# Optimization experiments

Hardware: AMD Instinct MI355X
Metric: run time of the kernel (lower is better)

## Reference

```python
import jax, jax.numpy as jnp
import numpy as np

DT = 0.01
DX = 1.0
DY = 1.0
NUM_STEPS = 10


def _diff(a, axis, h):
    """Central difference in the interior, one-sided at boundaries, along `axis`.
    a: [B, H, W]; returns same shape."""
    def sl(s):
        idx = [slice(None)] * a.ndim
        idx[axis] = s
        return a[tuple(idx)]
    left = (sl(slice(1, 2)) - sl(slice(0, 1))) / h            # one-sided forward at boundary 0
    interior = (sl(slice(2, None)) - sl(slice(None, -2))) / (2.0 * h)
    right = (sl(slice(-1, None)) - sl(slice(-2, -1))) / h     # one-sided backward at boundary -1
    return jnp.concatenate([left, interior, right], axis=axis)


def _diffusion_step(u, alpha, beta, aniso_x, aniso_y):
    # u: [B, H, W]; axis 1 = y, axis 2 = x (matches torch indexing)
    grad_x = _diff(u, axis=2, h=DX)
    grad_y = _diff(u, axis=1, h=DY)
    flux_x = (alpha * aniso_x) * grad_x   # scalars broadcast
    flux_y = (beta * aniso_y) * grad_y
    div_flux = _diff(flux_x, axis=2, h=DX) + _diff(flux_y, axis=1, h=DY)
    return u + DT * div_flux


def setup_inputs() -> dict:
    key = jax.random.key(0)
    k1, = jax.random.split(key, 1)
    u = jax.random.normal(k1, (64, 1, 512, 512), dtype=jnp.float32)
    ones = jnp.ones((1,), dtype=jnp.float32)
    return {
        "u": u,
        "alpha": ones * 0.5,
        "beta": ones * 0.5,
        "aniso_x": ones,
        "aniso_y": ones,
        "edge_strength": ones * 0.1,
    }


def reference(u, alpha, beta, aniso_x, aniso_y, edge_strength):
    # u: [B, 1, H, W] -> squeeze channel
    x = u[:, 0]                       # [B, H, W]
    x_orig = x

    def body(carry, _):
        return _diffusion_step(carry, alpha, beta, aniso_x, aniso_y), None

    x, _ = jax.lax.scan(body, x, None, length=NUM_STEPS)
    alpha_mix = jax.nn.sigmoid(edge_strength)   # shape (1,), broadcasts
    out = alpha_mix * x + (1.0 - alpha_mix) * x_orig
    return out[:, None]               # [B, 1, H, W]
```

## Files before the change

### kernel.cpp

```cpp
#include <hip/hip_runtime.h>
#include <math.h>

#define W 512
#define H 512
#define IMG (W * H)
#define LSTRIDE 84
#define WWORDS 2560
#define LWORDS (4 * WWORDS)

__host__ __device__ constexpr double dcoefd(int i, int j) {
    if (i == 0) return j == 0 ? 0.5 : j == 1 ? -1.0 : j == 2 ? 0.5 : 0.0;
    if (i == 1) return j == 0 ? 0.5 : j == 1 ? -0.75 : j == 3 ? 0.25 : 0.0;
    return j == i - 2 ? 0.25 : j == i ? -0.5 : j == i + 2 ? 0.25 : 0.0;
}

struct GhostT {
    float g[7][8];
    constexpr GhostT() : g{} {
        double v0[8] = {}, v1[8] = {}, v2[8] = {}, w0[8] = {}, w1r[8] = {}, w2r[8] = {};
        for (int j = 0; j < 8; ++j) { v0[j] = dcoefd(0, j); v1[j] = dcoefd(1, j); v2[j] = dcoefd(2, j); }
        for (int j = 0; j < 8; ++j) {
            double s0 = 0, s1 = 0, s2 = 0;
            for (int k = 0; k < 10; ++k) {
                s0 += dcoefd(0, k) * dcoefd(k, j);
                s1 += dcoefd(1, k) * dcoefd(k, j);
                s2 += dcoefd(2, k) * dcoefd(k, j);
            }
            w0[j] = s0; w1r[j] = s1; w2r[j] = s2;
        }
        double um1[8] = {}, um2[8] = {}, um3[8] = {}, um4[8] = {}, um5[8] = {}, um6[8] = {};
        double vm1[8] = {}, vm2[8] = {}, vm3[8] = {}, vm4[8] = {}, wm1[8] = {}, wm2[8] = {};
        for (int j = 0; j < 8; ++j) {
            um1[j] = 2.0 * (j == 0) - (j == 1);
            um2[j] = 4.0 * (j == 0) - 4.0 * (j == 1) + (j == 2);
            vm1[j] = 2 * v0[j] - v1[j];
            vm2[j] = 4 * v0[j] - 4 * v1[j] + v2[j];
            wm1[j] = 2 * w0[j] - w1r[j];
            wm2[j] = 4 * w0[j] - 4 * w1r[j] + w2r[j];
        }
        for (int j = 0; j < 8; ++j) {
            um3[j] = 4 * vm1[j] + 2 * um1[j] - (j == 1);
            um4[j] = 4 * vm2[j] + 2 * um2[j] - (j == 0);
            vm3[j] = 4 * wm1[j] + 2 * vm1[j] - v1[j];
            vm4[j] = 4 * wm2[j] + 2 * vm2[j] - v0[j];
        }
        for (int j = 0; j < 8; ++j) {
            um5[j] = 4 * vm3[j] + 2 * um3[j] - um1[j];
            um6[j] = 4 * vm4[j] + 2 * um4[j] - um2[j];
        }
        for (int j = 0; j < 8; ++j) {
            g[1][j] = (float)um1[j]; g[2][j] = (float)um2[j]; g[3][j] = (float)um3[j];
            g[4][j] = (float)um4[j]; g[5][j] = (float)um5[j]; g[6][j] = (float)um6[j];
        }
    }
};
constexpr GhostT GH{};

__device__ __forceinline__ float4 ld4(const float* p) {
    return *reinterpret_cast<const float4*>(p);
}
__device__ __forceinline__ float rfl(float x) {
    return __int_as_float(__builtin_amdgcn_readfirstlane(__float_as_int(x)));
}

struct Uni {
    float k1, k2, k3, m1, m2, n1;
    float wy1a, wy1b, wy2a, wy2b, wy2c, wy3a, wy3b, wy3c, wy3d;
    float am, iam;
};

template<int CLS, int RI>
__device__ __forceinline__ void row_lds(const Uni& U, const float* __restrict__ lbase,
                                        float acc[4][4]) {
    const float* rowp = lbase + 2 * RI * LSTRIDE;
    float u0a[4], t1a[4], t2a[4], t3a[4];
    if (CLS == 0) {
        const float4 m2 = ld4(rowp + 8);
        u0a[0] = m2.x; u0a[1] = m2.y; u0a[2] = m2.z; u0a[3] = m2.w;
    } else if (CLS <= 2) {
        const float4 m1 = ld4(rowp + 4);
        const float4 m2 = ld4(rowp + 8);
        const float4 m3 = ld4(rowp + 12);
        u0a[0] = m2.x; u0a[1] = m2.y; u0a[2] = m2.z; u0a[3] = m2.w;
        t1a[0] = m1.z + m2.z; t1a[1] = m1.w + m2.w;
        t1a[2] = m2.x + m3.x; t1a[3] = m2.y + m3.y;
        t2a[0] = m1.x + m3.x; t2a[1] = m1.y + m3.y;
        t2a[2] = m1.z + m3.z; t2a[3] = m1.w + m3.w;
    } else {
        const float4 m0 = ld4(rowp);
        const float4 m4 = ld4(rowp + 16);
        const float4 m1 = ld4(rowp + 4);
        const float4 m3 = ld4(rowp + 12);
        t3a[0] = m0.z + m3.z; t3a[1] = m0.w + m3.w;
        t3a[2] = m1.x + m4.x; t3a[3] = m1.y + m4.y;
        t2a[0] = m1.x + m3.x; t2a[1] = m1.y + m3.y;
        t2a[2] = m1.z + m3.z; t2a[3] = m1.w + m3.w;
        const float4 m2 = ld4(rowp + 8);
        t1a[0] = m1.z + m2.z; t1a[1] = m1.w + m2.w;
        t1a[2] = m2.x + m3.x; t1a[3] = m2.y + m3.y;
        u0a[0] = m2.x; u0a[1] = m2.y; u0a[2] = m2.z; u0a[3] = m2.w;
    }

    #pragma unroll
    for (int j = 0; j < 4; ++j) {
        const float u0 = u0a[j];
        const float M3v = 120.f * u0;
        float M2v = 0.f, M1v = 0.f, M0v = 0.f;
        if (CLS >= 1) {
            const float X1 = fmaf(0.25f, t1a[j], -0.5f * u0);
            M2v = fmaf(U.n1, X1, 45.f * u0);
            if (CLS >= 2) {
                const float X2 = fmaf(0.0625f, t2a[j], fmaf(-0.25f, t1a[j], 0.375f * u0));
                M1v = fmaf(U.m1, X1, fmaf(U.m2, X2, 10.f * u0));
                if (CLS >= 3) {
                    const float X3 = fmaf(1.f/64, t3a[j], fmaf(-6.f/64, t2a[j],
                                      fmaf(15.f/64, t1a[j], (-20.f/64) * u0)));
                    M0v = fmaf(U.k1, X1, fmaf(U.k2, X2, U.k3 * X3));
                }
            }
        }
        #pragma unroll
        for (int k = 0; k < 4; ++k) {
            const int dq = RI - 3 - k;
            const int ad = dq < 0 ? -dq : dq;
            if (ad > 3) continue;
            float a = acc[k][j];
            if (ad == 0) {
                a = fmaf(U.iam, u0, a);
                a += M0v;
                a = fmaf(U.wy1b, M1v, a);
                a = fmaf(U.wy2c, M2v, a);
                a = fmaf(U.wy3d, M3v, a);
            } else if (ad == 1) {
                a = fmaf(U.wy1a, M1v, a);
                a = fmaf(U.wy2b, M2v, a);
                a = fmaf(U.wy3c, M3v, a);
            } else if (ad == 2) {
                a = fmaf(U.wy2a, M2v, a);
                a = fmaf(U.wy3b, M3v, a);
            } else {
                a = fmaf(U.wy3a, M3v, a);
            }
            acc[k][j] = a;
        }
    }
}

__global__ __launch_bounds__(256) void fused_v17(
        const float* __restrict__ uin, float* __restrict__ outp,
        const float* __restrict__ alpha, const float* __restrict__ beta,
        const float* __restrict__ axp, const float* __restrict__ ayp,
        const float* __restrict__ es) {
    __shared__ float lds0[LWORDS];

    const unsigned bid = blockIdx.x;
    const unsigned swz = (bid & 7u) * (gridDim.x >> 3) + (bid >> 3);
    const unsigned img  = swz >> 6;
    const unsigned tile = swz & 63u;
    const int gx0 = (int)(tile & 7u) << 6;
    const int gy0 = (int)(tile >> 3) << 6;
    const float* __restrict__ p = uin + (size_t)img * IMG;
    float* __restrict__ q = outp + (size_t)img * IMG;

    const int tid = threadIdx.x;
    const int wid = tid >> 6, lane = tid & 63;
    const int WB = wid * WWORDS;
    const int wrow0 = 16 * wid - 6;

    #pragma unroll
    for (int t = 0; t < 10; ++t) {
        int idx = (t << 8) + (lane << 2);
        int lr  = (int)((unsigned)idx / 84u);
        int col = idx - lr * 84;
        int gy = gy0 + wrow0 + lr;
        gy = gy < 0 ? 0 : (gy > H - 1 ? H - 1 : gy);
        int gx = gx0 + col - 8;
        gx = gx < 0 ? 0 : (gx > W - 4 ? W - 4 : gx);
        const float* src = p + (size_t)gy * W + gx;
        __builtin_amdgcn_global_load_lds(
            (const __attribute__((address_space(1))) void*)src,
            (__attribute__((address_space(3))) void*)&lds0[WB + idx],
            16, 0, 0);
    }
    asm volatile("s_waitcnt vmcnt(0)" ::: "memory");

    if (gy0 == 0 && wid == 0 && lane < 20) {
        const int w0 = lane << 2;
        #pragma unroll
        for (int k = 1; k <= 6; ++k) {
            float4 a = {0.f, 0.f, 0.f, 0.f};
            #pragma unroll
            for (int j = 0; j < 8; ++j) {
                const float w = GH.g[k][j];
                if (w != 0.f) {
                    const float4 r = ld4(&lds0[WB + (6 + j) * LSTRIDE + w0]);
                    a.x = fmaf(w, r.x, a.x); a.y = fmaf(w, r.y, a.y);
                    a.z = fmaf(w, r.z, a.z); a.w = fmaf(w, r.w, a.w);
                }
            }
            *reinterpret_cast<float4*>(&lds0[WB + (6 - k) * LSTRIDE + w0]) = a;
        }
    }
    if (gy0 == H - 64 && wid == 3 && lane < 20) {
        const int w0 = lane << 2;
        #pragma unroll
        for (int k = 1; k <= 6; ++k) {
            float4 a = {0.f, 0.f, 0.f, 0.f};
            #pragma unroll
            for (int j = 0; j < 8; ++j) {
                const float w = GH.g[k][j];
                if (w != 0.f) {
                    const float4 r = ld4(&lds0[WB + (21 - j) * LSTRIDE + w0]);
                    a.x = fmaf(w, r.x, a.x); a.y = fmaf(w, r.y, a.y);
                    a.z = fmaf(w, r.z, a.z); a.w = fmaf(w, r.w, a.w);
                }
            }
            *reinterpret_cast<float4*>(&lds0[WB + (21 + k) * LSTRIDE + w0]) = a;
        }
    }

    if ((gx0 == 0 || gx0 == W - 64) && lane < 28) {
        float* rp = &lds0[WB + lane * LSTRIDE];
        #pragma unroll
        for (int k = 1; k <= 6; ++k) {
            float s = 0.f;
            #pragma unroll
            for (int j = 0; j < 8; ++j) {
                const float w = GH.g[k][j];
                if (w != 0.f) {
                    const float v = (gx0 == 0) ? rp[8 + j] : rp[71 - j];
                    s = fmaf(w, v, s);
                }
            }
            if (gx0 == 0) rp[8 - k] = s; else rp[71 + k] = s;
        }
    }

    const float sx = 0.01f * alpha[0] * axp[0];
    const float sy = 0.01f * beta[0]  * ayp[0];
    Uni U;
    U.k1 = rfl(10.f * sx);  U.k2 = rfl(45.f * sx * sx);  U.k3 = rfl(120.f * sx * sx * sx);
    U.m1 = rfl(90.f * sx);  U.m2 = rfl(360.f * sx * sx); U.n1 = rfl(360.f * sx);
    const float sy2 = sy * sy, sy3 = sy2 * sy;
    U.wy1a = rfl(0.25f * sy);    U.wy1b = rfl(-0.5f * sy);
    U.wy2a = rfl(0.0625f * sy2); U.wy2b = rfl(-0.25f * sy2); U.wy2c = rfl(0.375f * sy2);
    U.wy3a = rfl((1.f/64) * sy3);  U.wy3b = rfl((-6.f/64) * sy3);
    U.wy3c = rfl((15.f/64) * sy3); U.wy3d = rfl((-20.f/64) * sy3);
    const float amv = 1.f / (1.f + expf(-es[0]));
    U.am = rfl(amv); U.iam = rfl(1.f / amv);

    const int qc = tid & 15;
    const int gw = (tid >> 4) & 3;
    const int ly0 = ((gw >> 1) << 3) + (gw & 1);
    const int x0 = qc << 2;
    const float* lbase = &lds0[WB + ly0 * LSTRIDE + x0];

    float acc[4][4] = {};
    row_lds<0, 0>(U, lbase, acc);
    row_lds<1, 1>(U, lbase, acc);
    row_lds<2, 2>(U, lbase, acc);
    row_lds<3, 3>(U, lbase, acc);
    row_lds<3, 4>(U, lbase, acc);
    row_lds<3, 5>(U, lbase, acc);
    row_lds<3, 6>(U, lbase, acc);
    row_lds<2, 7>(U, lbase, acc);
    row_lds<1, 8>(U, lbase, acc);
    row_lds<0, 9>(U, lbase, acc);

    const int ybase = gy0 + 16 * wid + ly0;
    #pragma unroll
    for (int k = 0; k < 4; ++k) {
        const int Yo = ybase + 2 * k;
        float4 o;
        o.x = U.am * acc[k][0];
        o.y = U.am * acc[k][1];
        o.z = U.am * acc[k][2];
        o.w = U.am * acc[k][3];
        *reinterpret_cast<float4*>(q + (size_t)Yo * W + gx0 + x0) = o;
    }
}

extern "C" void kernel_launch(void* const* d_in, const int* in_sizes, int n_in,
                              void* d_out, int out_size, void* d_ws, size_t ws_size,
                              hipStream_t stream) {
    const float* u     = (const float*)d_in[0];
    const float* alpha = (const float*)d_in[1];
    const float* beta  = (const float*)d_in[2];
    const float* ax    = (const float*)d_in[3];
    const float* ay    = (const float*)d_in[4];
    const float* es    = (const float*)d_in[5];
    float* out = (float*)d_out;

    int nimg = in_sizes[0] / IMG;
    dim3 block(256);
    dim3 grid((unsigned)(nimg * 64));
    fused_v17<<<grid, block, 0, stream>>>(u, out, alpha, beta, ax, ay, es);
}
```

Before: 34.13 us.

## Process two horizontal tiles per block with double-buffered LDS staging

```diff
diff --git a/kernel.cpp b/kernel.cpp
--- a/kernel.cpp
+++ b/kernel.cpp
@@ -6,7 +6,7 @@
 #define IMG (W * H)
 #define LSTRIDE 84
 #define WWORDS 2560
-#define LWORDS (4 * WWORDS)
+#define LWORDS (8 * WWORDS)
 
 __host__ __device__ constexpr double dcoefd(int i, int j) {
     if (i == 0) return j == 0 ? 0.5 : j == 1 ? -1.0 : j == 2 ? 0.5 : 0.0;
@@ -146,27 +146,9 @@
     }
 }
 
-__global__ __launch_bounds__(256) void fused_v17(
-        const float* __restrict__ uin, float* __restrict__ outp,
-        const float* __restrict__ alpha, const float* __restrict__ beta,
-        const float* __restrict__ axp, const float* __restrict__ ayp,
-        const float* __restrict__ es) {
-    __shared__ float lds0[LWORDS];
-
-    const unsigned bid = blockIdx.x;
-    const unsigned swz = (bid & 7u) * (gridDim.x >> 3) + (bid >> 3);
-    const unsigned img  = swz >> 6;
-    const unsigned tile = swz & 63u;
-    const int gx0 = (int)(tile & 7u) << 6;
-    const int gy0 = (int)(tile >> 3) << 6;
-    const float* __restrict__ p = uin + (size_t)img * IMG;
-    float* __restrict__ q = outp + (size_t)img * IMG;
-
-    const int tid = threadIdx.x;
-    const int wid = tid >> 6, lane = tid & 63;
-    const int WB = wid * WWORDS;
-    const int wrow0 = 16 * wid - 6;
-
+__device__ __forceinline__ void stage_wave(const float* __restrict__ p,
+                                           float* ldsb, int gy0, int gx0,
+                                           int wrow0, int lane) {
     #pragma unroll
     for (int t = 0; t < 10; ++t) {
         int idx = (t << 8) + (lane << 2);
@@ -179,11 +161,13 @@
         const float* src = p + (size_t)gy * W + gx;
         __builtin_amdgcn_global_load_lds(
             (const __attribute__((address_space(1))) void*)src,
-            (__attribute__((address_space(3))) void*)&lds0[WB + idx],
+            (__attribute__((address_space(3))) void*)&ldsb[idx],
             16, 0, 0);
     }
-    asm volatile("s_waitcnt vmcnt(0)" ::: "memory");
-
+}
+
+__device__ __forceinline__ void ghost_wave(float* ldsb, int gy0, int gx0,
+                                           int wid, int lane) {
     if (gy0 == 0 && wid == 0 && lane < 20) {
         const int w0 = lane << 2;
         #pragma unroll
@@ -193,12 +177,12 @@
             for (int j = 0; j < 8; ++j) {
                 const float w = GH.g[k][j];
                 if (w != 0.f) {
-                    const float4 r = ld4(&lds0[WB + (6 + j) * LSTRIDE + w0]);
+                    const float4 r = ld4(&ldsb[(6 + j) * LSTRIDE + w0]);
                     a.x = fmaf(w, r.x, a.x); a.y = fmaf(w, r.y, a.y);
                     a.z = fmaf(w, r.z, a.z); a.w = fmaf(w, r.w, a.w);
                 }
             }
-            *reinterpret_cast<float4*>(&lds0[WB + (6 - k) * LSTRIDE + w0]) = a;
+            *reinterpret_cast<float4*>(&ldsb[(6 - k) * LSTRIDE + w0]) = a;
         }
     }
     if (gy0 == H - 64 && wid == 3 && lane < 20) {
@@ -210,17 +194,16 @@
             for (int j = 0; j < 8; ++j) {
                 const float w = GH.g[k][j];
                 if (w != 0.f) {
-                    const float4 r = ld4(&lds0[WB + (21 - j) * LSTRIDE + w0]);
+                    const float4 r = ld4(&ldsb[(21 - j) * LSTRIDE + w0]);
                     a.x = fmaf(w, r.x, a.x); a.y = fmaf(w, r.y, a.y);
                     a.z = fmaf(w, r.z, a.z); a.w = fmaf(w, r.w, a.w);
                 }
             }
-            *reinterpret_cast<float4*>(&lds0[WB + (21 + k) * LSTRIDE + w0]) = a;
-        }
-    }
-
+            *reinterpret_cast<float4*>(&ldsb[(21 + k) * LSTRIDE + w0]) = a;
+        }
+    }
     if ((gx0 == 0 || gx0 == W - 64) && lane < 28) {
-        float* rp = &lds0[WB + lane * LSTRIDE];
+        float* rp = &ldsb[lane * LSTRIDE];
         #pragma unroll
         for (int k = 1; k <= 6; ++k) {
             float s = 0.f;
@@ -235,6 +218,64 @@
             if (gx0 == 0) rp[8 - k] = s; else rp[71 + k] = s;
         }
     }
+}
+
+__device__ __forceinline__ void compute_wave(const Uni& U, const float* ldsb,
+                                             float* __restrict__ q,
+                                             int gy0, int gx0, int wid, int tid) {
+    const int qc = tid & 15;
+    const int gw = (tid >> 4) & 3;
+    const int ly0 = ((gw >> 1) << 3) + (gw & 1);
+    const int x0 = qc << 2;
+    const float* lbase = &ldsb[ly0 * LSTRIDE + x0];
+
+    float acc[4][4] = {};
+    row_lds<0, 0>(U, lbase, acc);
+    row_lds<1, 1>(U, lbase, acc);
+    row_lds<2, 2>(U, lbase, acc);
+    row_lds<3, 3>(U, lbase, acc);
+    row_lds<3, 4>(U, lbase, acc);
+    row_lds<3, 5>(U, lbase, acc);
+    row_lds<3, 6>(U, lbase, acc);
+    row_lds<2, 7>(U, lbase, acc);
+    row_lds<1, 8>(U, lbase, acc);
+    row_lds<0, 9>(U, lbase, acc);
+
+    const int ybase = gy0 + 16 * wid + ly0;
+    #pragma unroll
+    for (int k = 0; k < 4; ++k) {
+        const int Yo = ybase + 2 * k;
+        float4 o;
+        o.x = U.am * acc[k][0];
+        o.y = U.am * acc[k][1];
+        o.z = U.am * acc[k][2];
+        o.w = U.am * acc[k][3];
+        *reinterpret_cast<float4*>(q + (size_t)Yo * W + gx0 + x0) = o;
+    }
+}
+
+__global__ __launch_bounds__(256) void fused_v18(
+        const float* __restrict__ uin, float* __restrict__ outp,
+        const float* __restrict__ alpha, const float* __restrict__ beta,
+        const float* __restrict__ axp, const float* __restrict__ ayp,
+        const float* __restrict__ es) {
+    __shared__ float lds0[LWORDS];
+
+    const unsigned bid = blockIdx.x;
+    const unsigned swz = (bid & 7u) * (gridDim.x >> 3) + (bid >> 3);
+    const unsigned img = swz >> 5;
+    const unsigned pr  = swz & 31u;
+    const int gy0 = (int)(pr >> 2) << 6;
+    const int gxA = (int)(pr & 3u) << 7;
+    const int gxB = gxA + 64;
+    const float* __restrict__ p = uin + (size_t)img * IMG;
+    float* __restrict__ q = outp + (size_t)img * IMG;
+
+    const int tid = threadIdx.x;
+    const int wid = tid >> 6, lane = tid & 63;
+    const int wrow0 = 16 * wid - 6;
+    float* bufA = &lds0[(wid * 2 + 0) * WWORDS];
+    float* bufB = &lds0[(wid * 2 + 1) * WWORDS];
 
     const float sx = 0.01f * alpha[0] * axp[0];
     const float sy = 0.01f * beta[0]  * ayp[0];
@@ -249,35 +290,17 @@
     const float amv = 1.f / (1.f + expf(-es[0]));
     U.am = rfl(amv); U.iam = rfl(1.f / amv);
 
-    const int qc = tid & 15;
-    const int gw = (tid >> 4) & 3;
-    const int ly0 = ((gw >> 1) << 3) + (gw & 1);
-    const int x0 = qc << 2;
-    const float* lbase = &lds0[WB + ly0 * LSTRIDE + x0];
-
-    float acc[4][4] = {};
-    row_lds<0, 0>(U, lbase, acc);
-    row_lds<1, 1>(U, lbase, acc);
-    row_lds<2, 2>(U, lbase, acc);
-    row_lds<3, 3>(U, lbase, acc);
-    row_lds<3, 4>(U, lbase, acc);
-    row_lds<3, 5>(U, lbase, acc);
-    row_lds<3, 6>(U, lbase, acc);
-    row_lds<2, 7>(U, lbase, acc);
-    row_lds<1, 8>(U, lbase, acc);
-    row_lds<0, 9>(U, lbase, acc);
-
-    const int ybase = gy0 + 16 * wid + ly0;
-    #pragma unroll
-    for (int k = 0; k < 4; ++k) {
-        const int Yo = ybase + 2 * k;
-        float4 o;
-        o.x = U.am * acc[k][0];
-        o.y = U.am * acc[k][1];
-        o.z = U.am * acc[k][2];
-        o.w = U.am * acc[k][3];
-        *reinterpret_cast<float4*>(q + (size_t)Yo * W + gx0 + x0) = o;
-    }
+    stage_wave(p, bufA, gy0, gxA, wrow0, lane);
+    asm volatile("" ::: "memory");
+    stage_wave(p, bufB, gy0, gxB, wrow0, lane);
+
+    asm volatile("s_waitcnt vmcnt(10)" ::: "memory");
+    ghost_wave(bufA, gy0, gxA, wid, lane);
+    compute_wave(U, bufA, q, gy0, gxA, wid, tid);
+
+    asm volatile("s_waitcnt vmcnt(4)" ::: "memory");
+    ghost_wave(bufB, gy0, gxB, wid, lane);
+    compute_wave(U, bufB, q, gy0, gxB, wid, tid);
 }
 
 extern "C" void kernel_launch(void* const* d_in, const int* in_sizes, int n_in,
@@ -293,6 +316,6 @@
 
     int nimg = in_sizes[0] / IMG;
     dim3 block(256);
-    dim3 grid((unsigned)(nimg * 64));
-    fused_v17<<<grid, block, 0, stream>>>(u, out, alpha, beta, ax, ay, es);
-}
+    dim3 grid((unsigned)(nimg * 32));
+    fused_v18<<<grid, block, 0, stream>>>(u, out, alpha, beta, ax, ay, es);
+}
```

Result: slower. 35.02 us (+2.6%).
